# Kernel tuning notes

Measured on AMD Instinct MI355X. Metric: run time of the kernel, lower is better.

The kernel has to match this reference:

```python
import jax, jax.numpy as jnp
import numpy as np

B, L, D = 2, 4096, 128      # batch, seq_len, d_model
ED = 2 * D                  # d_inner (expand=2) = 256
N = 16                      # d_state
K = 4                       # d_conv
R = (D + 15) // 16          # dt_rank = 8
H = 2 * D                   # mlp hidden = 256


def setup_inputs() -> dict:
    key = jax.random.key(0)
    ks = jax.random.split(key, 20)
    s = 0.05
    inp = {
        "x": jax.random.normal(ks[0], (B, L, D), dtype=jnp.float32),
        # outer block LayerNorm (norm1)
        "norm1_g": jnp.ones((D,), jnp.float32),
        "norm1_b": jnp.zeros((D,), jnp.float32),
        # MambaLayer inner LayerNorm
        "inner_g": jnp.ones((D,), jnp.float32),
        "inner_b": jnp.zeros((D,), jnp.float32),
        # Mamba params
        "in_w": jax.random.normal(ks[1], (2 * ED, D), jnp.float32) * s,      # in_proj (no bias)
        "conv_w": jax.random.normal(ks[2], (ED, 1, K), jnp.float32) * s,     # depthwise conv
        "conv_b": jax.random.normal(ks[3], (ED,), jnp.float32) * s,
        "xproj_w": jax.random.normal(ks[4], (R + 2 * N, ED), jnp.float32) * s,  # x_proj (no bias)
        "dt_w": jax.random.normal(ks[5], (ED, R), jnp.float32) * s,
        "dt_b": jax.random.normal(ks[6], (ED,), jnp.float32) * s,
        "A_log": jnp.tile(jnp.log(jnp.arange(1, N + 1, dtype=jnp.float32)), (ED, 1)),  # [ED,N]
        "Dp": jnp.ones((ED,), jnp.float32),
        "out_w": jax.random.normal(ks[7], (D, ED), jnp.float32) * s,         # out_proj (no bias)
        # MLP
        "fc1_w": jax.random.normal(ks[8], (H, D), jnp.float32) * s,
        "fc1_b": jnp.zeros((H,), jnp.float32),
        "fc2_w": jax.random.normal(ks[9], (D, H), jnp.float32) * s,
        "fc2_b": jnp.zeros((D,), jnp.float32),
    }
    return inp


def _ln(x, g, b, eps=1e-5):
    m = jnp.mean(x, axis=-1, keepdims=True)
    v = jnp.mean((x - m) ** 2, axis=-1, keepdims=True)
    return (x - m) * jax.lax.rsqrt(v + eps) * g + b


def _mamba(x, in_w, conv_w, conv_b, xproj_w, dt_w, dt_b, A_log, Dp, out_w):
    # x: [B, L, D]
    xz = jnp.einsum('bld,ed->ble', x, in_w)          # [B,L,2*ED]
    u, z = jnp.split(xz, 2, axis=-1)                 # each [B,L,ED]
    # causal depthwise conv1d over L
    u_c = jnp.transpose(u, (0, 2, 1))                # [B,ED,L]
    u_c = jax.lax.conv_general_dilated(
        u_c, conv_w, window_strides=(1,), padding=[(K - 1, 0)],
        dimension_numbers=('NCH', 'OIH', 'NCH'), feature_group_count=ED)
    u = jax.nn.silu(jnp.transpose(u_c, (0, 2, 1)) + conv_b)   # [B,L,ED]
    # input-dependent dt, B, C
    dbc = jnp.einsum('ble,re->blr', u, xproj_w)      # [B,L,R+2N]
    dt, Bm, Cm = jnp.split(dbc, [R, R + N], axis=-1)
    delta = jax.nn.softplus(jnp.einsum('blr,er->ble', dt, dt_w) + dt_b)  # [B,L,ED]
    A = -jnp.exp(A_log)                              # [ED,N]
    deltaA = jnp.exp(jnp.einsum('ble,en->blen', delta, A))               # [B,L,ED,N]
    deltaBu = jnp.einsum('ble,bln,ble->blen', delta, Bm, u)              # [B,L,ED,N]
    # selective scan over L
    def step(h, inp):
        dA, dBu, Ct = inp                            # [B,ED,N],[B,ED,N],[B,N]
        h = dA * h + dBu
        y = jnp.einsum('ben,bn->be', h, Ct)
        return h, y
    h0 = jnp.zeros((B, ED, N), u.dtype)
    xs = (jnp.transpose(deltaA, (1, 0, 2, 3)),
          jnp.transpose(deltaBu, (1, 0, 2, 3)),
          jnp.transpose(Cm, (1, 0, 2)))
    _, ys = jax.lax.scan(step, h0, xs)               # [L,B,ED]
    y = jnp.transpose(ys, (1, 0, 2)) + u * Dp        # [B,L,ED]
    y = y * jax.nn.silu(z)
    return jnp.einsum('ble,de->bld', y, out_w)       # [B,L,D]


def reference(x, norm1_g, norm1_b, inner_g, inner_b, in_w, conv_w, conv_b,
              xproj_w, dt_w, dt_b, A_log, Dp, out_w, fc1_w, fc1_b, fc2_w, fc2_b):
    # attn branch: mamba(inner_LN(norm1(x)))
    a = _mamba(_ln(_ln(x, norm1_g, norm1_b), inner_g, inner_b),
               in_w, conv_w, conv_b, xproj_w, dt_w, dt_b, A_log, Dp, out_w)
    x = x + a
    # mlp branch (note: original applies norm1 again to updated x)
    h = _ln(x, norm1_g, norm1_b)
    h = jax.nn.gelu(jnp.einsum('bld,hd->blh', h, fc1_w) + fc1_b, approximate=False)
    h = jnp.einsum('blh,dh->bld', h, fc2_w) + fc2_b
    return x + h
```

## Files before the change

### kernel.cpp

```cpp
#include <hip/hip_runtime.h>
#include <hip/hip_bf16.h>
#include <math.h>

#define BB 2
#define LL 4096
#define DD 128
#define ED 256
#define NN 16
#define KK 4
#define RR 8
#define HH 256
#define NT (BB*LL)
#define NC 128
#define LC 32

#define LOG2E 1.4426950408889634f

typedef __attribute__((ext_vector_type(8))) short short8;
typedef __attribute__((ext_vector_type(8))) unsigned short ushort8v;
typedef __attribute__((ext_vector_type(4))) float floatx4;

__device__ __forceinline__ unsigned short f2bf(float f) {
  unsigned int b = __builtin_bit_cast(unsigned int, f);
  b += 0x7FFFu + ((b >> 16) & 1u);
  return (unsigned short)(b >> 16);
}

__device__ __forceinline__ float exp2_fast(float x) {
#if __has_builtin(__builtin_amdgcn_exp2f)
  return __builtin_amdgcn_exp2f(x);
#else
  return exp2f(x);
#endif
}

__device__ __forceinline__ ushort8v pack8(const float4& v0, const float4& v1) {
  ushort8v p;
  p[0]=f2bf(v0.x); p[1]=f2bf(v0.y); p[2]=f2bf(v0.z); p[3]=f2bf(v0.w);
  p[4]=f2bf(v1.x); p[5]=f2bf(v1.y); p[6]=f2bf(v1.z); p[7]=f2bf(v1.w);
  return p;
}

__global__ __launch_bounds__(512) void scan1h_k(
    const float* __restrict__ x,
    const float* __restrict__ g1, const float* __restrict__ b1,
    const float* __restrict__ g2, const float* __restrict__ b2,
    const float* __restrict__ in_w,
    const float* __restrict__ cw, const float* __restrict__ cb,
    const float* __restrict__ xpw,
    const float* __restrict__ dtw, const float* __restrict__ dtb,
    const float* __restrict__ A_log,
    float* __restrict__ uc, float* __restrict__ dbc,
    float* __restrict__ delta, float* __restrict__ gate,
    float* __restrict__ cA, float* __restrict__ cH) {
  __shared__ __align__(16) unsigned char SM[79888];
  auto Atile = reinterpret_cast<unsigned short(*)[136]>(SM);
  auto As    = reinterpret_cast<unsigned short(*)[264]>(SM);
  auto Wch   = reinterpret_cast<unsigned short(*)[136]>(SM + 16896);
  auto Bs    = reinterpret_cast<unsigned short(*)[264]>(SM + 16896);
  auto ubuf  = reinterpret_cast<float(*)[65]>(SM + 38016);
  auto sdbc  = reinterpret_cast<float(*)[40]>(SM + 38016);
  auto sus   = reinterpret_cast<float(*)[256]>(SM + 47120);

  const int c = blockIdx.x, b = blockIdx.y;
  const int tid = threadIdx.x;
  const int t0 = b*LL + c*LC;
  const int wave = tid >> 6, lane = tid & 63;
  const int quad = lane >> 4, l16 = lane & 15;

  {
    const int lr = tid >> 2, lk = (tid & 3) * 32;
    if (lr < 48) {
      if (lr < 35 && !(c == 0 && lr < 3)) {
        const float* Ap = x + (size_t)(t0 - 3 + lr)*DD + lk;
        float4 av[8];
        float s = 0.f, sq = 0.f;
        #pragma unroll
        for (int g = 0; g < 8; g++) {
          av[g] = *(const float4*)(Ap + g*4);
          s  += av[g].x + av[g].y + av[g].z + av[g].w;
          sq += av[g].x*av[g].x + av[g].y*av[g].y + av[g].z*av[g].z + av[g].w*av[g].w;
        }
        s += __shfl_xor(s, 1);  s += __shfl_xor(s, 2);
        sq += __shfl_xor(sq, 1); sq += __shfl_xor(sq, 2);
        const float m1 = s * (1.f/128.f);
        const float rs1 = rsqrtf(sq*(1.f/128.f) - m1*m1 + 1e-5f);
        float s2 = 0.f, sq2 = 0.f;
        #pragma unroll
        for (int g = 0; g < 8; g++) {
          const float4 gg = *(const float4*)(g1 + lk + g*4);
          const float4 bb = *(const float4*)(b1 + lk + g*4);
          av[g].x = (av[g].x - m1)*rs1*gg.x + bb.x;
          av[g].y = (av[g].y - m1)*rs1*gg.y + bb.y;
          av[g].z = (av[g].z - m1)*rs1*gg.z + bb.z;
          av[g].w = (av[g].w - m1)*rs1*gg.w + bb.w;
          s2  += av[g].x + av[g].y + av[g].z + av[g].w;
          sq2 += av[g].x*av[g].x + av[g].y*av[g].y + av[g].z*av[g].z + av[g].w*av[g].w;
        }
        s2 += __shfl_xor(s2, 1);  s2 += __shfl_xor(s2, 2);
        sq2 += __shfl_xor(sq2, 1); sq2 += __shfl_xor(sq2, 2);
        const float m2 = s2 * (1.f/128.f);
        const float rs2 = rsqrtf(sq2*(1.f/128.f) - m2*m2 + 1e-5f);
        #pragma unroll
        for (int g = 0; g < 4; g++) {
          const float4 ga = *(const float4*)(g2 + lk + g*8);
          const float4 gb = *(const float4*)(g2 + lk + g*8 + 4);
          const float4 ba = *(const float4*)(b2 + lk + g*8);
          const float4 bbv= *(const float4*)(b2 + lk + g*8 + 4);
          ushort8v pa;
          pa[0] = f2bf((av[2*g].x   - m2)*rs2*ga.x + ba.x);
          pa[1] = f2bf((av[2*g].y   - m2)*rs2*ga.y + ba.y);
          pa[2] = f2bf((av[2*g].z   - m2)*rs2*ga.z + ba.z);
          pa[3] = f2bf((av[2*g].w   - m2)*rs2*ga.w + ba.w);
          pa[4] = f2bf((av[2*g+1].x - m2)*rs2*gb.x + bbv.x);
          pa[5] = f2bf((av[2*g+1].y - m2)*rs2*gb.y + bbv.y);
          pa[6] = f2bf((av[2*g+1].z - m2)*rs2*gb.z + bbv.z);
          pa[7] = f2bf((av[2*g+1].w - m2)*rs2*gb.w + bbv.w);
          *(ushort8v*)&Atile[lr][lk + g*8] = pa;
        }
      } else {
        const ushort8v zz = {};
        #pragma unroll
        for (int g = 0; g < 4; g++) *(ushort8v*)&Atile[lr][lk + g*8] = zz;
      }
    }
  }
  __syncthreads();

  const int nt_w = wave & 3;
  const int mlo  = (wave < 4) ? 0 : 16;
  short8 af0[4], af1[4];
  #pragma unroll
  for (int ks = 0; ks < 4; ks++) {
    af0[ks] = *(const short8*)&Atile[mlo + l16][ks*32 + quad*8];
    if (wave < 4) af1[ks] = *(const short8*)&Atile[32 + l16][ks*32 + quad*8];
  }
  __syncthreads();

  {
    const int wr = tid >> 3;
    const int wseg = (tid & 7) * 16;
    float4 wv[4];
    #pragma unroll
    for (int g = 0; g < 4; g++)
      wv[g] = *(const float4*)(in_w + (size_t)wr*DD + wseg + g*4);
    for (int nc = 0; nc < 8; nc++) {
      *(ushort8v*)&Wch[wr][wseg]     = pack8(wv[0], wv[1]);
      *(ushort8v*)&Wch[wr][wseg + 8] = pack8(wv[2], wv[3]);
      __syncthreads();
      if (nc < 7) {
        const float* wp = in_w + (size_t)((nc+1)*64 + wr)*DD + wseg;
        #pragma unroll
        for (int g = 0; g < 4; g++) wv[g] = *(const float4*)(wp + g*4);
      }
      floatx4 acc0 = {}, acc1 = {};
      #pragma unroll
      for (int ks = 0; ks < 4; ks++) {
        short8 bv = *(const short8*)&Wch[nt_w*16 + l16][ks*32 + quad*8];
        acc0 = __builtin_amdgcn_mfma_f32_16x16x32_bf16(af0[ks], bv, acc0, 0, 0, 0);
        if (wave < 4)
          acc1 = __builtin_amdgcn_mfma_f32_16x16x32_bf16(af1[ks], bv, acc1, 0, 0, 0);
      }
      const int coll = nt_w*16 + l16;
      if (nc < 4) {
        #pragma unroll
        for (int rr = 0; rr < 4; rr++)
          ubuf[mlo + quad*4 + rr][coll] = acc0[rr];
        if (wave < 4) {
          #pragma unroll
          for (int rr = 0; rr < 4; rr++) {
            const int m1 = 32 + quad*4 + rr;
            if (m1 < 35) ubuf[m1][coll] = acc1[rr];
          }
        }
      } else {
        const int gcol = (nc-4)*64 + coll;
        #pragma unroll
        for (int rr = 0; rr < 4; rr++) {
          const int m0 = mlo + quad*4 + rr;
          if (m0 >= 3) {
            const float v = acc0[rr];
            gate[(size_t)(t0 + m0 - 3)*ED + gcol] = v / (1.f + __expf(-v));
          }
        }
        if (wave < 4) {
          #pragma unroll
          for (int rr = 0; rr < 4; rr++) {
            const int m1 = 32 + quad*4 + rr;
            if (m1 < 35) {
              const float v = acc1[rr];
              gate[(size_t)(t0 + m1 - 3)*ED + gcol] = v / (1.f + __expf(-v));
            }
          }
        }
      }
      __syncthreads();
      if (nc < 4) {
        const int chl = tid & 63, tg = tid >> 6;
        const int ch = nc*64 + chl;
        const float4 w = *(const float4*)(cw + ch*4);
        const float cbe = cb[ch];
        float v0 = ubuf[tg*4 + 0][chl];
        float v1 = ubuf[tg*4 + 1][chl];
        float v2 = ubuf[tg*4 + 2][chl];
        #pragma unroll
        for (int k = 0; k < 4; k++) {
          const float cur = ubuf[tg*4 + 3 + k][chl];
          const float a = cbe + v0*w.x + v1*w.y + v2*w.z + cur*w.w;
          const float s = a / (1.f + __expf(-a));
          const int i = tg*4 + k;
          As[i][ch] = f2bf(s);
          sus[i][ch] = s;
          uc[(size_t)(t0+i)*ED + ch] = s;
          v0 = v1; v1 = v2; v2 = cur;
        }
      }
    }
  }
  __syncthreads();

  #pragma unroll
  for (int p = 0; p < 3; p++) {
    const int idx = p*512 + tid;
    if (idx < 1280) {
      const int row = idx >> 5;
      const int col = (idx & 31) * 8;
      const float4 v0 = *(const float4*)(xpw + (size_t)row*ED + col);
      const float4 v1 = *(const float4*)(xpw + (size_t)row*ED + col + 4);
      *(ushort8v*)&Bs[row][col] = pack8(v0, v1);
    }
  }
  __syncthreads();

  {
    const int mt = wave & 1, nt = wave >> 1;
    if (wave < 6) {
      const int jn = (nt == 2) ? 24 : nt*16;
      floatx4 acc = {};
      #pragma unroll
      for (int ks = 0; ks < 8; ks++) {
        const int ko = ks*32 + quad*8;
        short8 a  = *(const short8*)&As[mt*16 + l16][ko];
        short8 bv = *(const short8*)&Bs[jn + l16][ko];
        acc = __builtin_amdgcn_mfma_f32_16x16x32_bf16(a, bv, acc, 0, 0, 0);
      }
      const int n = jn + l16;
      if (nt < 2 || l16 >= 8) {
        #pragma unroll
        for (int rr = 0; rr < 4; rr++) {
          const int m = mt*16 + quad*4 + rr;
          sdbc[m][n] = acc[rr];
          dbc[(size_t)(t0 + m)*40 + n] = acc[rr];
        }
      }
    }
  }
  __syncthreads();

  {
    const int e = tid >> 1, half = tid & 1;
    const int n0 = half * 8;
    const float4 dw0 = *(const float4*)(dtw + e*RR);
    const float4 dw1 = *(const float4*)(dtw + e*RR + 4);
    const float db = dtb[e];
    const float4 a0 = *(const float4*)(A_log + e*NN + n0);
    const float4 a1 = *(const float4*)(A_log + e*NN + n0 + 4);
    float Aen[8] = {-__expf(a0.x)*LOG2E, -__expf(a0.y)*LOG2E,
                    -__expf(a0.z)*LOG2E, -__expf(a0.w)*LOG2E,
                    -__expf(a1.x)*LOG2E, -__expf(a1.y)*LOG2E,
                    -__expf(a1.z)*LOG2E, -__expf(a1.w)*LOG2E};
    float h[8] = {};
    float sumd = 0.f;
    for (int t = 0; t < LC; t++) {
      const float4 q0 = *(const float4*)&sdbc[t][0];
      const float4 q1 = *(const float4*)&sdbc[t][4];
      const float aa = db
          + q0.x*dw0.x + q0.y*dw0.y + q0.z*dw0.z + q0.w*dw0.w
          + q1.x*dw1.x + q1.y*dw1.y + q1.z*dw1.z + q1.w*dw1.w;
      const float dv = (aa > 20.f) ? aa : log1pf(__expf(aa));
      if (half == 0) delta[(size_t)(t0+t)*ED + e] = dv;
      const float du = dv * sus[t][e];
      const float4 B0 = *(const float4*)&sdbc[t][RR + n0];
      const float4 B1 = *(const float4*)&sdbc[t][RR + n0 + 4];
      const float Bv[8] = {B0.x,B0.y,B0.z,B0.w,B1.x,B1.y,B1.z,B1.w};
      sumd += dv;
      #pragma unroll
      for (int j = 0; j < 8; j++)
        h[j] = exp2_fast(dv * Aen[j])*h[j] + Bv[j]*du;
    }
    const size_t base = (((size_t)c*BB + b)*ED + e)*NN + n0;
    *(float4*)(cA + base)     = make_float4(exp2_fast(sumd*Aen[0]), exp2_fast(sumd*Aen[1]),
                                            exp2_fast(sumd*Aen[2]), exp2_fast(sumd*Aen[3]));
    *(float4*)(cA + base + 4) = make_float4(exp2_fast(sumd*Aen[4]), exp2_fast(sumd*Aen[5]),
                                            exp2_fast(sumd*Aen[6]), exp2_fast(sumd*Aen[7]));
    *(float4*)(cH + base)     = make_float4(h[0], h[1], h[2], h[3]);
    *(float4*)(cH + base + 4) = make_float4(h[4], h[5], h[6], h[7]);
  }
}

__global__ __launch_bounds__(256) void scan2p_k(float* __restrict__ cA,
    const float* __restrict__ cH) {
  const int gt = blockIdx.x*256 + threadIdx.x;
  const int scan = gt >> 2;
  const int seg  = gt & 3;
  const int lane = threadIdx.x & 63;
  const int lb   = lane & ~3;
  const int b = scan >> 12;
  const size_t base = (size_t)b*ED*NN + (scan & 4095);
  const int c0 = seg * 32;

  float ap = 1.f, hs = 0.f;
  for (int g = 0; g < 2; g++) {
    float av[16], hv[16];
    #pragma unroll
    for (int i = 0; i < 16; i++) {
      const size_t idx = (size_t)(c0 + g*16 + i)*(BB*ED*NN) + base;
      av[i] = cA[idx]; hv[i] = cH[idx];
    }
    #pragma unroll
    for (int i = 0; i < 16; i++) {
      hs = av[i]*hs + hv[i];
      ap *= av[i];
    }
  }
  float h = 0.f;
  #pragma unroll
  for (int k = 0; k < 3; k++) {
    const float ak = __shfl(ap, lb + k);
    const float hk = __shfl(hs, lb + k);
    if (seg > k) h = ak*h + hk;
  }
  for (int g = 0; g < 2; g++) {
    float av[16], hv[16];
    #pragma unroll
    for (int i = 0; i < 16; i++) {
      const size_t idx = (size_t)(c0 + g*16 + i)*(BB*ED*NN) + base;
      av[i] = cA[idx]; hv[i] = cH[idx];
    }
    #pragma unroll
    for (int i = 0; i < 16; i++) {
      const size_t idx = (size_t)(c0 + g*16 + i)*(BB*ED*NN) + base;
      cA[idx] = h;
      h = av[i]*h + hv[i];
    }
  }
}

__global__ __launch_bounds__(1024) void tail7_k(
    const float* __restrict__ gate, const float* __restrict__ delta,
    const float* __restrict__ uc, const float* __restrict__ dbc,
    const float* __restrict__ cP, const float* __restrict__ A_log,
    const float* __restrict__ Dpv, const float* __restrict__ x,
    const float* __restrict__ g1, const float* __restrict__ b1,
    const float* __restrict__ out_w, const float* __restrict__ fc1_w,
    const float* __restrict__ fc1_b, const float* __restrict__ fc2_w,
    const float* __restrict__ fc2_b, float* __restrict__ out) {
  __shared__ __align__(16) unsigned short BigW[34816];
  __shared__ __align__(16) unsigned short Au[32][264];
  __shared__ float xs[32][132];
  __shared__ float sbc[32][32];

  const int c = blockIdx.x, b = blockIdx.y;
  const int t0 = b*LL + c*LC;
  const int tid = threadIdx.x;
  const int wave = tid >> 6, lane = tid & 63;
  const int quad = lane >> 4, l16 = lane & 15;

  if (tid < 256) {
    const int row = tid >> 3, c4 = (tid & 7) * 4;
    *(float4*)&sbc[row][c4] = *(const float4*)(dbc + (size_t)(t0 + row)*40 + RR + c4);
  }
  __syncthreads();

  {
    const int r = tid >> 3, k0 = (tid & 7) * 32;
    const float* wp = out_w + (size_t)r*ED + k0;
    #pragma unroll
    for (int g = 0; g < 4; g++) {
      const float4 v0 = *(const float4*)(wp + g*8);
      const float4 v1 = *(const float4*)(wp + g*8 + 4);
      *(ushort8v*)&BigW[(size_t)r*264 + k0 + g*8] = pack8(v0, v1);
    }
  }

  {
    const int e = tid >> 2, q = tid & 3;
    const int n0 = q * 4;
    float Aen[4], h[4];
    {
      const float4 a0 = *(const float4*)(A_log + e*NN + n0);
      Aen[0]=-__expf(a0.x)*LOG2E; Aen[1]=-__expf(a0.y)*LOG2E;
      Aen[2]=-__expf(a0.z)*LOG2E; Aen[3]=-__expf(a0.w)*LOG2E;
      const float4 h0 = *(const float4*)(cP + (((size_t)c*BB + b)*ED + e)*NN + n0);
      h[0]=h0.x; h[1]=h0.y; h[2]=h0.z; h[3]=h0.w;
    }
    const float Dpe = Dpv[e];
    float pd[8], pu[8], pg[8];
    #pragma unroll
    for (int i = 0; i < 8; i++) {
      pd[i] = delta[(size_t)(t0+i)*ED + e];
      pu[i] = uc[(size_t)(t0+i)*ED + e];
      pg[i] = gate[(size_t)(t0+i)*ED + e];
    }
    for (int g4 = 0; g4 < 4; g4++) {
      float cd[8], cu[8], cg[8];
      #pragma unroll
      for (int i = 0; i < 8; i++) { cd[i]=pd[i]; cu[i]=pu[i]; cg[i]=pg[i]; }
      if (g4 < 3) {
        const int tn = t0 + (g4+1)*8;
        #pragma unroll
        for (int i = 0; i < 8; i++) {
          pd[i] = delta[(size_t)(tn+i)*ED + e];
          pu[i] = uc[(size_t)(tn+i)*ED + e];
          pg[i] = gate[(size_t)(tn+i)*ED + e];
        }
      }
      #pragma unroll
      for (int i = 0; i < 8; i++) {
        const int t = g4*8 + i;
        const float dv = cd[i];
        const float uv = cu[i];
        const float du = dv * uv;
        const float4 B0 = *(const float4*)&sbc[t][n0];
        const float4 C0 = *(const float4*)&sbc[t][16 + n0];
        const float Bv[4] = {B0.x,B0.y,B0.z,B0.w};
        const float Cv[4] = {C0.x,C0.y,C0.z,C0.w};
        float part = 0.f;
        #pragma unroll
        for (int j = 0; j < 4; j++) {
          h[j] = exp2_fast(dv * Aen[j])*h[j] + Bv[j]*du;
          part += h[j]*Cv[j];
        }
        part += __shfl_xor(part, 1);
        part += __shfl_xor(part, 2);
        if (q == 0)
          Au[t][e] = f2bf((part + uv*Dpe) * cg[i]);
      }
    }
  }
  __syncthreads();

  {
    const int mi = (wave & 1) * 16;
    const int wn = (wave >> 1) * 16;
    floatx4 acc = {};
    #pragma unroll
    for (int ks = 0; ks < 8; ks++) {
      const int ko = ks*32 + quad*8;
      short8 a  = *(const short8*)&Au[mi + l16][ko];
      short8 bv = *(const short8*)&BigW[(size_t)(wn + l16)*264 + ko];
      acc = __builtin_amdgcn_mfma_f32_16x16x32_bf16(a, bv, acc, 0, 0, 0);
    }
    const int n = wn + l16;
    #pragma unroll
    for (int r = 0; r < 4; r++) {
      const int m = mi + quad*4 + r;
      xs[m][n] = acc[r] + x[(size_t)(t0 + m)*DD + n];
    }
  }
  __syncthreads();

  if (tid < 512) {
    const int lr = tid >> 4, le = (tid & 15) * 8;
    float vv[8];
    float s = 0.f, sq = 0.f;
    #pragma unroll
    for (int i = 0; i < 8; i++) {
      vv[i] = xs[lr][le + i];
      s += vv[i]; sq += vv[i]*vv[i];
    }
    s += __shfl_xor(s, 1);  s += __shfl_xor(s, 2);
    s += __shfl_xor(s, 4);  s += __shfl_xor(s, 8);
    sq += __shfl_xor(sq, 1); sq += __shfl_xor(sq, 2);
    sq += __shfl_xor(sq, 4); sq += __shfl_xor(sq, 8);
    const float mean = s * (1.f/128.f);
    const float rs = rsqrtf(sq*(1.f/128.f) - mean*mean + 1e-5f);
    ushort8v p;
    #pragma unroll
    for (int i = 0; i < 8; i++)
      p[i] = f2bf((vv[i] - mean)*rs*g1[le + i] + b1[le + i]);
    *(ushort8v*)&Au[lr][le] = p;
  }
  {
    const int r = tid >> 2, k0 = (tid & 3) * 32;
    const float* wp = fc1_w + (size_t)r*DD + k0;
    #pragma unroll
    for (int g = 0; g < 4; g++) {
      const float4 v0 = *(const float4*)(wp + g*8);
      const float4 v1 = *(const float4*)(wp + g*8 + 4);
      *(ushort8v*)&BigW[(size_t)r*136 + k0 + g*8] = pack8(v0, v1);
    }
  }
  __syncthreads();

  {
    const int mi = (wave & 1) * 16;
    const int wn = (wave >> 1) * 32;
    floatx4 acc[2] = {};
    #pragma unroll
    for (int ks = 0; ks < 4; ks++) {
      const int ko = ks*32 + quad*8;
      short8 a  = *(const short8*)&Au[mi + l16][ko];
      short8 b0 = *(const short8*)&BigW[(size_t)(wn +      l16)*136 + ko];
      short8 b1 = *(const short8*)&BigW[(size_t)(wn + 16 + l16)*136 + ko];
      acc[0] = __builtin_amdgcn_mfma_f32_16x16x32_bf16(a, b0, acc[0], 0, 0, 0);
      acc[1] = __builtin_amdgcn_mfma_f32_16x16x32_bf16(a, b1, acc[1], 0, 0, 0);
    }
    __syncthreads();
    #pragma unroll
    for (int f = 0; f < 2; f++) {
      const int n = wn + f*16 + l16;
      const float bn = fc1_b[n];
      #pragma unroll
      for (int r = 0; r < 4; r++) {
        const int m = mi + quad*4 + r;
        float v = acc[f][r] + bn;
        v = 0.5f*v*(1.f + erff(v*0.70710678118f));
        Au[m][n] = f2bf(v);
      }
    }
  }
  {
    const int r = tid >> 3, k0 = (tid & 7) * 32;
    const float* wp = fc2_w + (size_t)r*HH + k0;
    #pragma unroll
    for (int g = 0; g < 4; g++) {
      const float4 v0 = *(const float4*)(wp + g*8);
      const float4 v1 = *(const float4*)(wp + g*8 + 4);
      *(ushort8v*)&BigW[(size_t)r*264 + k0 + g*8] = pack8(v0, v1);
    }
  }
  __syncthreads();

  {
    const int mi = (wave & 1) * 16;
    const int wn = (wave >> 1) * 16;
    floatx4 acc = {};
    #pragma unroll
    for (int ks = 0; ks < 8; ks++) {
      const int ko = ks*32 + quad*8;
      short8 a  = *(const short8*)&Au[mi + l16][ko];
      short8 bv = *(const short8*)&BigW[(size_t)(wn + l16)*264 + ko];
      acc = __builtin_amdgcn_mfma_f32_16x16x32_bf16(a, bv, acc, 0, 0, 0);
    }
    const int n = wn + l16;
    const float bn = fc2_b[n];
    #pragma unroll
    for (int r = 0; r < 4; r++) {
      const int m = mi + quad*4 + r;
      out[(size_t)(t0 + m)*DD + n] = acc[r] + bn + xs[m][n];
    }
  }
}

extern "C" void kernel_launch(void* const* d_in, const int* in_sizes, int n_in,
                              void* d_out, int out_size, void* d_ws, size_t ws_size,
                              hipStream_t stream) {
  const float* x      = (const float*)d_in[0];
  const float* n1g    = (const float*)d_in[1];
  const float* n1b    = (const float*)d_in[2];
  const float* ing    = (const float*)d_in[3];
  const float* inb    = (const float*)d_in[4];
  const float* in_w   = (const float*)d_in[5];
  const float* conv_w = (const float*)d_in[6];
  const float* conv_b = (const float*)d_in[7];
  const float* xproj_w= (const float*)d_in[8];
  const float* dt_w   = (const float*)d_in[9];
  const float* dt_b   = (const float*)d_in[10];
  const float* A_log  = (const float*)d_in[11];
  const float* Dpv    = (const float*)d_in[12];
  const float* out_w  = (const float*)d_in[13];
  const float* fc1_w  = (const float*)d_in[14];
  const float* fc1_b  = (const float*)d_in[15];
  const float* fc2_w  = (const float*)d_in[16];
  const float* fc2_b  = (const float*)d_in[17];
  float* out = (float*)d_out;

  float* ws    = (float*)d_ws;
  float* uc    = ws;
  float* dbc   = uc    + (size_t)NT*ED;
  float* delta = dbc   + (size_t)NT*40;
  float* gate  = delta + (size_t)NT*ED;
  float* cA    = gate  + (size_t)NT*ED;
  float* cH    = cA    + (size_t)NC*BB*ED*NN;

  scan1h_k<<<dim3(NC, BB), 512, 0, stream>>>(x, n1g, n1b, ing, inb, in_w,
                                             conv_w, conv_b, xproj_w, dt_w, dt_b,
                                             A_log, uc, dbc, delta, gate, cA, cH);
  scan2p_k<<<(4*BB*ED*NN)/256, 256, 0, stream>>>(cA, cH);
  tail7_k<<<dim3(NC, BB), 1024, 0, stream>>>(gate, delta, uc, dbc, cA, A_log, Dpv,
                                             x, n1g, n1b, out_w, fc1_w, fc1_b,
                                             fc2_w, fc2_b, out);
}
```

Baseline: 165.1 us.

## Stage in_proj weights in two 256-row halves instead of eight 64-row chunks

The in_proj GEMM in the first kernel now loads 256 weight rows at a time into a larger LDS buffer rather than iterating over eight 64-row chunks, with each wave computing a 48x32 tile across three M-tiles. This replaces eight sync-separated GEMM and conv rounds with two large phases, and the depthwise conv then covers all 256 channels in one pass. The cost is shared memory rising to about 156 KB per block, which limits blocks per CU to one and may reduce occupancy. It also drops the register prefetch of the next weight chunk, so weight loads are no longer overlapped with the MFMA work.

```diff
diff --git a/kernel.cpp b/kernel.cpp
--- a/kernel.cpp
+++ b/kernel.cpp
@@ -41,7 +41,7 @@
   return p;
 }
 
-__global__ __launch_bounds__(512) void scan1h_k(
+__global__ __launch_bounds__(512) void scan1i_k(
     const float* __restrict__ x,
     const float* __restrict__ g1, const float* __restrict__ b1,
     const float* __restrict__ g2, const float* __restrict__ b2,
@@ -53,14 +53,14 @@
     float* __restrict__ uc, float* __restrict__ dbc,
     float* __restrict__ delta, float* __restrict__ gate,
     float* __restrict__ cA, float* __restrict__ cH) {
-  __shared__ __align__(16) unsigned char SM[79888];
+  __shared__ __align__(16) unsigned char SM[156256];
   auto Atile = reinterpret_cast<unsigned short(*)[136]>(SM);
   auto As    = reinterpret_cast<unsigned short(*)[264]>(SM);
   auto Wch   = reinterpret_cast<unsigned short(*)[136]>(SM + 16896);
   auto Bs    = reinterpret_cast<unsigned short(*)[264]>(SM + 16896);
-  auto ubuf  = reinterpret_cast<float(*)[65]>(SM + 38016);
-  auto sdbc  = reinterpret_cast<float(*)[40]>(SM + 38016);
-  auto sus   = reinterpret_cast<float(*)[256]>(SM + 47120);
+  auto ubuf  = reinterpret_cast<float(*)[257]>(SM + 86528);
+  auto sdbc  = reinterpret_cast<float(*)[40]>(SM + 86528);
+  auto sus   = reinterpret_cast<float(*)[256]>(SM + 123488);
 
   const int c = blockIdx.x, b = blockIdx.y;
   const int tid = threadIdx.x;
@@ -127,95 +127,109 @@
   }
   __syncthreads();
 
-  const int nt_w = wave & 3;
-  const int mlo  = (wave < 4) ? 0 : 16;
-  short8 af0[4], af1[4];
+  short8 af[3][4];
   #pragma unroll
-  for (int ks = 0; ks < 4; ks++) {
-    af0[ks] = *(const short8*)&Atile[mlo + l16][ks*32 + quad*8];
-    if (wave < 4) af1[ks] = *(const short8*)&Atile[32 + l16][ks*32 + quad*8];
-  }
-  __syncthreads();
-
-  {
-    const int wr = tid >> 3;
-    const int wseg = (tid & 7) * 16;
-    float4 wv[4];
-    #pragma unroll
-    for (int g = 0; g < 4; g++)
-      wv[g] = *(const float4*)(in_w + (size_t)wr*DD + wseg + g*4);
-    for (int nc = 0; nc < 8; nc++) {
-      *(ushort8v*)&Wch[wr][wseg]     = pack8(wv[0], wv[1]);
-      *(ushort8v*)&Wch[wr][wseg + 8] = pack8(wv[2], wv[3]);
-      __syncthreads();
-      if (nc < 7) {
-        const float* wp = in_w + (size_t)((nc+1)*64 + wr)*DD + wseg;
-        #pragma unroll
-        for (int g = 0; g < 4; g++) wv[g] = *(const float4*)(wp + g*4);
-      }
-      floatx4 acc0 = {}, acc1 = {};
-      #pragma unroll
-      for (int ks = 0; ks < 4; ks++) {
-        short8 bv = *(const short8*)&Wch[nt_w*16 + l16][ks*32 + quad*8];
-        acc0 = __builtin_amdgcn_mfma_f32_16x16x32_bf16(af0[ks], bv, acc0, 0, 0, 0);
-        if (wave < 4)
-          acc1 = __builtin_amdgcn_mfma_f32_16x16x32_bf16(af1[ks], bv, acc1, 0, 0, 0);
-      }
-      const int coll = nt_w*16 + l16;
-      if (nc < 4) {
-        #pragma unroll
-        for (int rr = 0; rr < 4; rr++)
-          ubuf[mlo + quad*4 + rr][coll] = acc0[rr];
-        if (wave < 4) {
-          #pragma unroll
-          for (int rr = 0; rr < 4; rr++) {
-            const int m1 = 32 + quad*4 + rr;
-            if (m1 < 35) ubuf[m1][coll] = acc1[rr];
-          }
-        }
-      } else {
-        const int gcol = (nc-4)*64 + coll;
-        #pragma unroll
-        for (int rr = 0; rr < 4; rr++) {
-          const int m0 = mlo + quad*4 + rr;
-          if (m0 >= 3) {
-            const float v = acc0[rr];
-            gate[(size_t)(t0 + m0 - 3)*ED + gcol] = v / (1.f + __expf(-v));
-          }
-        }
-        if (wave < 4) {
-          #pragma unroll
-          for (int rr = 0; rr < 4; rr++) {
-            const int m1 = 32 + quad*4 + rr;
-            if (m1 < 35) {
-              const float v = acc1[rr];
-              gate[(size_t)(t0 + m1 - 3)*ED + gcol] = v / (1.f + __expf(-v));
-            }
-          }
-        }
-      }
-      __syncthreads();
-      if (nc < 4) {
-        const int chl = tid & 63, tg = tid >> 6;
-        const int ch = nc*64 + chl;
-        const float4 w = *(const float4*)(cw + ch*4);
-        const float cbe = cb[ch];
-        float v0 = ubuf[tg*4 + 0][chl];
-        float v1 = ubuf[tg*4 + 1][chl];
-        float v2 = ubuf[tg*4 + 2][chl];
-        #pragma unroll
-        for (int k = 0; k < 4; k++) {
-          const float cur = ubuf[tg*4 + 3 + k][chl];
-          const float a = cbe + v0*w.x + v1*w.y + v2*w.z + cur*w.w;
-          const float s = a / (1.f + __expf(-a));
-          const int i = tg*4 + k;
-          As[i][ch] = f2bf(s);
-          sus[i][ch] = s;
-          uc[(size_t)(t0+i)*ED + ch] = s;
-          v0 = v1; v1 = v2; v2 = cur;
-        }
-      }
-    }
+  for (int mt = 0; mt < 3; mt++)
+    #pragma unroll
+    for (int ks = 0; ks < 4; ks++)
+      af[mt][ks] = *(const short8*)&Atile[mt*16 + l16][ks*32 + quad*8];
+
+  const int wr = tid >> 1;
+  const int wk = (tid & 1) * 64;
+
+  {
+    const float* wp = in_w + (size_t)wr*DD + wk;
+    #pragma unroll
+    for (int g = 0; g < 8; g++) {
+      const float4 v0 = *(const float4*)(wp + g*8);
+      const float4 v1 = *(const float4*)(wp + g*8 + 4);
+      *(ushort8v*)&Wch[wr][wk + g*8] = pack8(v0, v1);
+    }
+  }
+  __syncthreads();
+
+  {
+    floatx4 acc[3][2] = {};
+    #pragma unroll
+    for (int ks = 0; ks < 4; ks++) {
+      const int ko = ks*32 + quad*8;
+      short8 b0 = *(const short8*)&Wch[(2*wave)*16 + l16][ko];
+      short8 b1 = *(const short8*)&Wch[(2*wave+1)*16 + l16][ko];
+      #pragma unroll
+      for (int mt = 0; mt < 3; mt++) {
+        acc[mt][0] = __builtin_amdgcn_mfma_f32_16x16x32_bf16(af[mt][ks], b0, acc[mt][0], 0, 0, 0);
+        acc[mt][1] = __builtin_amdgcn_mfma_f32_16x16x32_bf16(af[mt][ks], b1, acc[mt][1], 0, 0, 0);
+      }
+    }
+    const int coll0 = 32*wave + l16;
+    #pragma unroll
+    for (int mt = 0; mt < 3; mt++)
+      #pragma unroll
+      for (int rr = 0; rr < 4; rr++) {
+        const int m = mt*16 + quad*4 + rr;
+        if (m < 35) {
+          ubuf[m][coll0]      = acc[mt][0][rr];
+          ubuf[m][coll0 + 16] = acc[mt][1][rr];
+        }
+      }
+  }
+  __syncthreads();
+
+  {
+    const int ch = tid & 255, tg = tid >> 8;
+    const int i0 = tg * 16;
+    const float4 w = *(const float4*)(cw + ch*4);
+    const float cbe = cb[ch];
+    float v0 = ubuf[i0][ch], v1 = ubuf[i0+1][ch], v2 = ubuf[i0+2][ch];
+    #pragma unroll
+    for (int k = 0; k < 16; k++) {
+      const float cur = ubuf[i0+3+k][ch];
+      const float a = cbe + v0*w.x + v1*w.y + v2*w.z + cur*w.w;
+      const float s = a / (1.f + __expf(-a));
+      const int i = i0 + k;
+      As[i][ch] = f2bf(s);
+      sus[i][ch] = s;
+      uc[(size_t)(t0+i)*ED + ch] = s;
+      v0 = v1; v1 = v2; v2 = cur;
+    }
+  }
+  {
+    const float* wp = in_w + (size_t)(256 + wr)*DD + wk;
+    #pragma unroll
+    for (int g = 0; g < 8; g++) {
+      const float4 v0 = *(const float4*)(wp + g*8);
+      const float4 v1 = *(const float4*)(wp + g*8 + 4);
+      *(ushort8v*)&Wch[wr][wk + g*8] = pack8(v0, v1);
+    }
+  }
+  __syncthreads();
+
+  {
+    floatx4 acc[3][2] = {};
+    #pragma unroll
+    for (int ks = 0; ks < 4; ks++) {
+      const int ko = ks*32 + quad*8;
+      short8 b0 = *(const short8*)&Wch[(2*wave)*16 + l16][ko];
+      short8 b1 = *(const short8*)&Wch[(2*wave+1)*16 + l16][ko];
+      #pragma unroll
+      for (int mt = 0; mt < 3; mt++) {
+        acc[mt][0] = __builtin_amdgcn_mfma_f32_16x16x32_bf16(af[mt][ks], b0, acc[mt][0], 0, 0, 0);
+        acc[mt][1] = __builtin_amdgcn_mfma_f32_16x16x32_bf16(af[mt][ks], b1, acc[mt][1], 0, 0, 0);
+      }
+    }
+    const int gcol = 32*wave + l16;
+    #pragma unroll
+    for (int mt = 0; mt < 3; mt++)
+      #pragma unroll
+      for (int rr = 0; rr < 4; rr++) {
+        const int m = mt*16 + quad*4 + rr;
+        if (m >= 3 && m < 35) {
+          const float va = acc[mt][0][rr];
+          const float vb = acc[mt][1][rr];
+          gate[(size_t)(t0 + m - 3)*ED + gcol]      = va / (1.f + __expf(-va));
+          gate[(size_t)(t0 + m - 3)*ED + gcol + 16] = vb / (1.f + __expf(-vb));
+        }
+      }
   }
   __syncthreads();
 
@@ -584,7 +598,7 @@
   float* cA    = gate  + (size_t)NT*ED;
   float* cH    = cA    + (size_t)NC*BB*ED*NN;
 
-  scan1h_k<<<dim3(NC, BB), 512, 0, stream>>>(x, n1g, n1b, ing, inb, in_w,
+  scan1i_k<<<dim3(NC, BB), 512, 0, stream>>>(x, n1g, n1b, ing, inb, in_w,
                                              conv_w, conv_b, xproj_w, dt_w, dt_b,
                                              A_log, uc, dbc, delta, gate, cA, cH);
   scan2p_k<<<(4*BB*ED*NN)/256, 256, 0, stream>>>(cA, cH);
```

Measured after the change: 167.4 us. Within noise of the previous version (+1.4%).

## Halve scan-phase chunk length to double blocks and raise occupancy

Applied to the files above, without the earlier changes.

Changes the first kernel to process 16-token chunks instead of 32, launching twice as many blocks with smaller shared memory and a launch bound that allows four blocks per CU. The MFMA tiling is reworked so each wave handles one 16x16 tile. The carry scan now combines 8 segments per scan, and the tail kernel reads carries at every other chunk boundary. This trades more chunk-carry work and redundant conv-halo loads of the in_proj weights for more parallelism in the input projection and chunk scan phase.

```diff
diff --git a/kernel.cpp b/kernel.cpp
--- a/kernel.cpp
+++ b/kernel.cpp
@@ -13,6 +13,8 @@
 #define NT (BB*LL)
 #define NC 128
 #define LC 32
+#define NCS 256
+#define LCS 16
 
 #define LOG2E 1.4426950408889634f
 
@@ -41,7 +43,7 @@
   return p;
 }
 
-__global__ __launch_bounds__(512) void scan1h_k(
+__global__ __launch_bounds__(512, 4) void scan1j_k(
     const float* __restrict__ x,
     const float* __restrict__ g1, const float* __restrict__ b1,
     const float* __restrict__ g2, const float* __restrict__ b2,
@@ -53,25 +55,25 @@
     float* __restrict__ uc, float* __restrict__ dbc,
     float* __restrict__ delta, float* __restrict__ gate,
     float* __restrict__ cA, float* __restrict__ cH) {
-  __shared__ __align__(16) unsigned char SM[79888];
+  __shared__ __align__(16) unsigned char SM[51152];
   auto Atile = reinterpret_cast<unsigned short(*)[136]>(SM);
   auto As    = reinterpret_cast<unsigned short(*)[264]>(SM);
-  auto Wch   = reinterpret_cast<unsigned short(*)[136]>(SM + 16896);
-  auto Bs    = reinterpret_cast<unsigned short(*)[264]>(SM + 16896);
-  auto ubuf  = reinterpret_cast<float(*)[65]>(SM + 38016);
-  auto sdbc  = reinterpret_cast<float(*)[40]>(SM + 38016);
-  auto sus   = reinterpret_cast<float(*)[256]>(SM + 47120);
-
-  const int c = blockIdx.x, b = blockIdx.y;
+  auto Wch   = reinterpret_cast<unsigned short(*)[136]>(SM + 8704);
+  auto Bs    = reinterpret_cast<unsigned short(*)[264]>(SM + 8704);
+  auto ubuf  = reinterpret_cast<float(*)[65]>(SM + 29824);
+  auto sdbc  = reinterpret_cast<float(*)[40]>(SM + 29824);
+  auto sus   = reinterpret_cast<float(*)[256]>(SM + 34768);
+
+  const int c2 = blockIdx.x, b = blockIdx.y;
   const int tid = threadIdx.x;
-  const int t0 = b*LL + c*LC;
+  const int t0 = b*LL + c2*LCS;
   const int wave = tid >> 6, lane = tid & 63;
   const int quad = lane >> 4, l16 = lane & 15;
 
   {
     const int lr = tid >> 2, lk = (tid & 3) * 32;
-    if (lr < 48) {
-      if (lr < 35 && !(c == 0 && lr < 3)) {
+    if (lr < 32) {
+      if (lr < 19 && !(c2 == 0 && lr < 3)) {
         const float* Ap = x + (size_t)(t0 - 3 + lr)*DD + lk;
         float4 av[8];
         float s = 0.f, sq = 0.f;
@@ -127,19 +129,17 @@
   }
   __syncthreads();
 
-  const int nt_w = wave & 3;
-  const int mlo  = (wave < 4) ? 0 : 16;
-  short8 af0[4], af1[4];
+  short8 af[2][4];
   #pragma unroll
-  for (int ks = 0; ks < 4; ks++) {
-    af0[ks] = *(const short8*)&Atile[mlo + l16][ks*32 + quad*8];
-    if (wave < 4) af1[ks] = *(const short8*)&Atile[32 + l16][ks*32 + quad*8];
-  }
-  __syncthreads();
+  for (int mt = 0; mt < 2; mt++)
+    #pragma unroll
+    for (int ks = 0; ks < 4; ks++)
+      af[mt][ks] = *(const short8*)&Atile[mt*16 + l16][ks*32 + quad*8];
 
   {
     const int wr = tid >> 3;
     const int wseg = (tid & 7) * 16;
+    const int mt_w = wave & 1, nt_w = wave >> 1;
     float4 wv[4];
     #pragma unroll
     for (int g = 0; g < 4; g++)
@@ -153,44 +153,27 @@
         #pragma unroll
         for (int g = 0; g < 4; g++) wv[g] = *(const float4*)(wp + g*4);
       }
-      floatx4 acc0 = {}, acc1 = {};
+      floatx4 acc = {};
       #pragma unroll
       for (int ks = 0; ks < 4; ks++) {
         short8 bv = *(const short8*)&Wch[nt_w*16 + l16][ks*32 + quad*8];
-        acc0 = __builtin_amdgcn_mfma_f32_16x16x32_bf16(af0[ks], bv, acc0, 0, 0, 0);
-        if (wave < 4)
-          acc1 = __builtin_amdgcn_mfma_f32_16x16x32_bf16(af1[ks], bv, acc1, 0, 0, 0);
+        acc = __builtin_amdgcn_mfma_f32_16x16x32_bf16(af[mt_w][ks], bv, acc, 0, 0, 0);
       }
       const int coll = nt_w*16 + l16;
       if (nc < 4) {
         #pragma unroll
-        for (int rr = 0; rr < 4; rr++)
-          ubuf[mlo + quad*4 + rr][coll] = acc0[rr];
-        if (wave < 4) {
-          #pragma unroll
-          for (int rr = 0; rr < 4; rr++) {
-            const int m1 = 32 + quad*4 + rr;
-            if (m1 < 35) ubuf[m1][coll] = acc1[rr];
-          }
+        for (int rr = 0; rr < 4; rr++) {
+          const int m = mt_w*16 + quad*4 + rr;
+          if (m < 19) ubuf[m][coll] = acc[rr];
         }
       } else {
         const int gcol = (nc-4)*64 + coll;
         #pragma unroll
         for (int rr = 0; rr < 4; rr++) {
-          const int m0 = mlo + quad*4 + rr;
-          if (m0 >= 3) {
-            const float v = acc0[rr];
-            gate[(size_t)(t0 + m0 - 3)*ED + gcol] = v / (1.f + __expf(-v));
-          }
-        }
-        if (wave < 4) {
-          #pragma unroll
-          for (int rr = 0; rr < 4; rr++) {
-            const int m1 = 32 + quad*4 + rr;
-            if (m1 < 35) {
-              const float v = acc1[rr];
-              gate[(size_t)(t0 + m1 - 3)*ED + gcol] = v / (1.f + __expf(-v));
-            }
+          const int m = mt_w*16 + quad*4 + rr;
+          if (m >= 3 && m < 19) {
+            const float v = acc[rr];
+            gate[(size_t)(t0 + m - 3)*ED + gcol] = v / (1.f + __expf(-v));
           }
         }
       }
@@ -200,15 +183,14 @@
         const int ch = nc*64 + chl;
         const float4 w = *(const float4*)(cw + ch*4);
         const float cbe = cb[ch];
-        float v0 = ubuf[tg*4 + 0][chl];
-        float v1 = ubuf[tg*4 + 1][chl];
-        float v2 = ubuf[tg*4 + 2][chl];
-        #pragma unroll
-        for (int k = 0; k < 4; k++) {
-          const float cur = ubuf[tg*4 + 3 + k][chl];
+        const int i0 = tg*2;
+        float v0 = ubuf[i0][chl], v1 = ubuf[i0+1][chl], v2 = ubuf[i0+2][chl];
+        #pragma unroll
+        for (int k = 0; k < 2; k++) {
+          const float cur = ubuf[i0+3+k][chl];
           const float a = cbe + v0*w.x + v1*w.y + v2*w.z + cur*w.w;
           const float s = a / (1.f + __expf(-a));
-          const int i = tg*4 + k;
+          const int i = i0 + k;
           As[i][ch] = f2bf(s);
           sus[i][ch] = s;
           uc[(size_t)(t0+i)*ED + ch] = s;
@@ -232,26 +214,23 @@
   }
   __syncthreads();
 
-  {
-    const int mt = wave & 1, nt = wave >> 1;
-    if (wave < 6) {
-      const int jn = (nt == 2) ? 24 : nt*16;
-      floatx4 acc = {};
+  if (wave < 3) {
+    const int jn = (wave == 2) ? 24 : wave*16;
+    floatx4 acc = {};
+    #pragma unroll
+    for (int ks = 0; ks < 8; ks++) {
+      const int ko = ks*32 + quad*8;
+      short8 a  = *(const short8*)&As[l16][ko];
+      short8 bv = *(const short8*)&Bs[jn + l16][ko];
+      acc = __builtin_amdgcn_mfma_f32_16x16x32_bf16(a, bv, acc, 0, 0, 0);
+    }
+    const int n = jn + l16;
+    if (wave < 2 || l16 >= 8) {
       #pragma unroll
-      for (int ks = 0; ks < 8; ks++) {
-        const int ko = ks*32 + quad*8;
-        short8 a  = *(const short8*)&As[mt*16 + l16][ko];
-        short8 bv = *(const short8*)&Bs[jn + l16][ko];
-        acc = __builtin_amdgcn_mfma_f32_16x16x32_bf16(a, bv, acc, 0, 0, 0);
-      }
-      const int n = jn + l16;
-      if (nt < 2 || l16 >= 8) {
-        #pragma unroll
-        for (int rr = 0; rr < 4; rr++) {
-          const int m = mt*16 + quad*4 + rr;
-          sdbc[m][n] = acc[rr];
-          dbc[(size_t)(t0 + m)*40 + n] = acc[rr];
-        }
+      for (int rr = 0; rr < 4; rr++) {
+        const int m = quad*4 + rr;
+        sdbc[m][n] = acc[rr];
+        dbc[(size_t)(t0 + m)*40 + n] = acc[rr];
       }
     }
   }
@@ -271,7 +250,7 @@
                     -__expf(a1.z)*LOG2E, -__expf(a1.w)*LOG2E};
     float h[8] = {};
     float sumd = 0.f;
-    for (int t = 0; t < LC; t++) {
+    for (int t = 0; t < LCS; t++) {
       const float4 q0 = *(const float4*)&sdbc[t][0];
       const float4 q1 = *(const float4*)&sdbc[t][4];
       const float aa = db
@@ -288,7 +267,7 @@
       for (int j = 0; j < 8; j++)
         h[j] = exp2_fast(dv * Aen[j])*h[j] + Bv[j]*du;
     }
-    const size_t base = (((size_t)c*BB + b)*ED + e)*NN + n0;
+    const size_t base = (((size_t)c2*BB + b)*ED + e)*NN + n0;
     *(float4*)(cA + base)     = make_float4(exp2_fast(sumd*Aen[0]), exp2_fast(sumd*Aen[1]),
                                             exp2_fast(sumd*Aen[2]), exp2_fast(sumd*Aen[3]));
     *(float4*)(cA + base + 4) = make_float4(exp2_fast(sumd*Aen[4]), exp2_fast(sumd*Aen[5]),
@@ -298,13 +277,13 @@
   }
 }
 
-__global__ __launch_bounds__(256) void scan2p_k(float* __restrict__ cA,
+__global__ __launch_bounds__(256) void scan2p8_k(float* __restrict__ cA,
     const float* __restrict__ cH) {
   const int gt = blockIdx.x*256 + threadIdx.x;
-  const int scan = gt >> 2;
-  const int seg  = gt & 3;
+  const int scan = gt >> 3;
+  const int seg  = gt & 7;
   const int lane = threadIdx.x & 63;
-  const int lb   = lane & ~3;
+  const int lb   = lane & ~7;
   const int b = scan >> 12;
   const size_t base = (size_t)b*ED*NN + (scan & 4095);
   const int c0 = seg * 32;
@@ -325,7 +304,7 @@
   }
   float h = 0.f;
   #pragma unroll
-  for (int k = 0; k < 3; k++) {
+  for (int k = 0; k < 7; k++) {
     const float ak = __shfl(ap, lb + k);
     const float hk = __shfl(hs, lb + k);
     if (seg > k) h = ak*h + hk;
@@ -346,7 +325,7 @@
   }
 }
 
-__global__ __launch_bounds__(1024) void tail7_k(
+__global__ __launch_bounds__(1024) void tail8_k(
     const float* __restrict__ gate, const float* __restrict__ delta,
     const float* __restrict__ uc, const float* __restrict__ dbc,
     const float* __restrict__ cP, const float* __restrict__ A_log,
@@ -391,7 +370,7 @@
       const float4 a0 = *(const float4*)(A_log + e*NN + n0);
       Aen[0]=-__expf(a0.x)*LOG2E; Aen[1]=-__expf(a0.y)*LOG2E;
       Aen[2]=-__expf(a0.z)*LOG2E; Aen[3]=-__expf(a0.w)*LOG2E;
-      const float4 h0 = *(const float4*)(cP + (((size_t)c*BB + b)*ED + e)*NN + n0);
+      const float4 h0 = *(const float4*)(cP + (((size_t)(2*c)*BB + b)*ED + e)*NN + n0);
       h[0]=h0.x; h[1]=h0.y; h[2]=h0.z; h[3]=h0.w;
     }
     const float Dpe = Dpv[e];
@@ -582,13 +561,13 @@
   float* delta = dbc   + (size_t)NT*40;
   float* gate  = delta + (size_t)NT*ED;
   float* cA    = gate  + (size_t)NT*ED;
-  float* cH    = cA    + (size_t)NC*BB*ED*NN;
-
-  scan1h_k<<<dim3(NC, BB), 512, 0, stream>>>(x, n1g, n1b, ing, inb, in_w,
-                                             conv_w, conv_b, xproj_w, dt_w, dt_b,
-                                             A_log, uc, dbc, delta, gate, cA, cH);
-  scan2p_k<<<(4*BB*ED*NN)/256, 256, 0, stream>>>(cA, cH);
-  tail7_k<<<dim3(NC, BB), 1024, 0, stream>>>(gate, delta, uc, dbc, cA, A_log, Dpv,
+  float* cH    = cA    + (size_t)NCS*BB*ED*NN;
+
+  scan1j_k<<<dim3(NCS, BB), 512, 0, stream>>>(x, n1g, n1b, ing, inb, in_w,
+                                              conv_w, conv_b, xproj_w, dt_w, dt_b,
+                                              A_log, uc, dbc, delta, gate, cA, cH);
+  scan2p8_k<<<(8*BB*ED*NN)/256, 256, 0, stream>>>(cA, cH);
+  tail8_k<<<dim3(NC, BB), 1024, 0, stream>>>(gate, delta, uc, dbc, cA, A_log, Dpv,
                                              x, n1g, n1b, out_w, fc1_w, fc1_b,
                                              fc2_w, fc2_b, out);
 }
```

Result: slower. 189.0 us (+14.5%).
